# Performance work log

Measured on AMD Instinct MI355X. Metric: run time of the kernel, lower is better.

Reference implementation:

```python
import jax, jax.numpy as jnp
import numpy as np

B = 4096      # graphs per batch
V = 32        # vertices per graph
F = 16        # num_atom_types (input node features)
NB = 8        # num_bond_types (edge feature dim)
C = 128       # conv_dim
E_PER = 256   # random edges per graph
NEG_SLOPE = 0.2


def setup_inputs() -> dict:
    rng = np.random.default_rng(0)
    N = B * V
    # random intra-graph edges (duplicates are fine; softmax handles them)
    off = (np.arange(B, dtype=np.int64) * V)[:, None]
    src = (rng.integers(0, V, (B, E_PER)) + off).ravel()
    dst = (rng.integers(0, V, (B, E_PER)) + off).ravel()
    bond = rng.integers(0, NB, src.shape[0])
    eattr = np.zeros((src.shape[0], NB), dtype=np.float32)
    eattr[np.arange(src.shape[0]), bond] = 1.0
    # self loops with edge_attr = per-target-node mean (PyG fill_value='mean')
    sums = np.zeros((N, NB), dtype=np.float64)
    np.add.at(sums, dst, eattr)
    cnt = np.bincount(dst, minlength=N).astype(np.float64)
    loop_attr = (sums / np.maximum(cnt, 1.0)[:, None]).astype(np.float32)
    loops = np.arange(N, dtype=np.int64)
    edge_index = np.stack([np.concatenate([src, loops]),
                           np.concatenate([dst, loops])])  # [2, E]
    edge_attr = np.concatenate([eattr, loop_attr], axis=0)  # [E, NB]

    key = jax.random.key(0)
    ks = jax.random.split(key, 8)
    inp = {
        "x": jax.random.normal(ks[0], (N, F), jnp.float32),
        "edge_index": jnp.asarray(edge_index),
        "edge_attr": jnp.asarray(edge_attr),
        "W_lin": jax.random.normal(ks[1], (F, C), jnp.float32) / np.sqrt(F),
        "att_src": jax.random.normal(ks[2], (C,), jnp.float32) / np.sqrt(C),
        "att_dst": jax.random.normal(ks[3], (C,), jnp.float32) / np.sqrt(C),
        "att_edge": jax.random.normal(ks[4], (C,), jnp.float32) / np.sqrt(C),
        "W_edge": jax.random.normal(ks[5], (NB, C), jnp.float32) / np.sqrt(NB),
        "b_gat": jnp.zeros((C,), jnp.float32),
        "W_out": jax.random.normal(ks[6], (C, 1), jnp.float32) / np.sqrt(C),
        "b_out": jnp.zeros((1,), jnp.float32),
        "num_graphs": B,
    }
    return inp


def reference(x, edge_index, edge_attr, W_lin, att_src, att_dst, att_edge,
              W_edge, b_gat, W_out, b_out, num_graphs):
    N = x.shape[0]
    src, dst = edge_index[0], edge_index[1]
    h = x @ W_lin                           # [N, C] node transform
    a_src = h @ att_src                     # [N]
    a_dst = h @ att_dst                     # [N]
    a_edge = (edge_attr @ W_edge) @ att_edge  # [E]
    alpha = jax.nn.leaky_relu(a_src[src] + a_dst[dst] + a_edge, NEG_SLOPE)
    # segment softmax over incoming edges of each dst node
    m = jax.ops.segment_max(alpha, dst, num_segments=N)
    m = jnp.where(jnp.isfinite(m), m, 0.0)
    ex = jnp.exp(alpha - m[dst])
    denom = jax.ops.segment_sum(ex, dst, num_segments=N)
    w = ex / denom[dst]                     # [E] attention weights
    msg = h[src] * w[:, None]               # [E, C]
    out_nodes = jax.ops.segment_sum(msg, dst, num_segments=N) + b_gat  # [N, C]
    gf = out_nodes.reshape(num_graphs, -1, out_nodes.shape[-1]).mean(axis=1)  # [B, C]
    out = gf @ W_out + b_out                # [B, 1]
    return (out, gf)
```

## Files before the change

kernel.cpp:

```cpp
#include <hip/hip_runtime.h>


#define BB   4096
#define VV   32
#define FF   16
#define NBB  8
#define CC   128
#define EPER 256
constexpr int NTOT  = BB * VV;
constexpr int ERAND = BB * EPER;
constexpr int ETOT  = ERAND + NTOT;
constexpr float SLOPE = 0.2f;

__launch_bounds__(256, 4)
__global__ void gnn_all(const float* __restrict__ x,
                        const int*   __restrict__ eidx,
                        const float* __restrict__ eattr,
                        const float* __restrict__ W_lin,
                        const float* __restrict__ att_src,
                        const float* __restrict__ att_dst,
                        const float* __restrict__ att_edge,
                        const float* __restrict__ W_edge,
                        const float* __restrict__ b_gat,
                        const float* __restrict__ W_out,
                        const float* __restrict__ b_out,
                        float* __restrict__ out,
                        float* __restrict__ gf_out)
{
  const int t    = threadIdx.x;
  const int lane = t & 63;
  const int wave = __builtin_amdgcn_readfirstlane(t) >> 6;
  const int g    = blockIdx.x * 4 + wave;
  const int half = lane >> 5;
  const int v    = lane & 31;

  __shared__ float2 s_a[4][VV];
  __shared__ float  s_den[4][VV];
  __shared__ float  s_r[4][VV];
  __shared__ float2 s_uv[4][FF];
  __shared__ __align__(16) float s_we[4][NBB];
  __shared__ float  s_xt[4][FF * 33];
  __shared__ __align__(16) float s_y[4][FF];

  float4 xa, xb;
  {
    const float* xp = x + (size_t)(g * VV + v) * FF + half * 8;
    xa = ((const float4*)xp)[0]; xb = ((const float4*)xp)[1];
  }
  int es[4], ed[4];
  float4 ea0[4], ea1[4];
  #pragma unroll
  for (int k = 0; k < 4; ++k) {
    const int e = g * EPER + 64 * k + lane;
    es[k] = eidx[e] - g * VV;
    ed[k] = eidx[ETOT + e] - g * VV;
    const float4* ap = (const float4*)(eattr + (size_t)e * NBB);
    ea0[k] = ap[0]; ea1[k] = ap[1];
  }
  float4 la0 = {0,0,0,0}, la1 = {0,0,0,0};
  if (half) {
    const float4* lp = (const float4*)(eattr + (size_t)(ERAND + g * VV + v) * NBB);
    la0 = lp[0]; la1 = lp[1];
  }

  {
    const int fu = lane & 15, q = lane >> 4;
    const float4* wr = (const float4*)(W_lin + fu * CC + q * 32);
    const float4* as = (const float4*)(att_src + q * 32);
    const float4* ad = (const float4*)(att_dst + q * 32);
    float us = 0.f, ud = 0.f;
    #pragma unroll
    for (int j = 0; j < 8; ++j) {
      const float4 w = wr[j], a = as[j], d = ad[j];
      us += w.x*a.x + w.y*a.y + w.z*a.z + w.w*a.w;
      ud += w.x*d.x + w.y*d.y + w.z*d.z + w.w*d.w;
    }
    us += __shfl_xor(us, 16); us += __shfl_xor(us, 32);
    ud += __shfl_xor(ud, 16); ud += __shfl_xor(ud, 32);
    if (lane < FF) s_uv[wave][lane] = make_float2(us, ud);
  }
  if (!half) {
    const int f8 = v & 7, oct = v >> 3;
    const float4* wr = (const float4*)(W_edge + f8 * CC + oct * 32);
    const float4* ae = (const float4*)(att_edge + oct * 32);
    float pe = 0.f;
    #pragma unroll
    for (int j = 0; j < 8; ++j) {
      const float4 w = wr[j], a = ae[j];
      pe += w.x*a.x + w.y*a.y + w.z*a.z + w.w*a.w;
    }
    pe += __shfl_xor(pe, 8); pe += __shfl_xor(pe, 16);
    if (v < NBB) s_we[wave][v] = pe;
  }

  float a0 = 0.f, a1 = 0.f;
  {
    const float xr[8] = {xa.x, xa.y, xa.z, xa.w, xb.x, xb.y, xb.z, xb.w};
    #pragma unroll
    for (int j = 0; j < 8; ++j) {
      const float2 u = s_uv[wave][half * 8 + j];
      a0 += xr[j] * u.x; a1 += xr[j] * u.y;
    }
  }
  a0 += __shfl_xor(a0, 32); a1 += __shfl_xor(a1, 32);
  if (!half) {
    s_a[wave][v] = make_float2(a0, a1);
    s_den[wave][v] = 0.f; s_r[wave][v] = 0.f;
  }
  __threadfence_block();

  const float4 w03 = *(const float4*)&s_we[wave][0];
  const float4 w47 = *(const float4*)&s_we[wave][4];
  float ex[5];
  #pragma unroll
  for (int k = 0; k < 4; ++k) {
    const float2 A = s_a[wave][es[k]];
    const float2 D = s_a[wave][ed[k]];
    const float aed = ea0[k].x*w03.x + ea0[k].y*w03.y + ea0[k].z*w03.z + ea0[k].w*w03.w
                    + ea1[k].x*w47.x + ea1[k].y*w47.y + ea1[k].z*w47.z + ea1[k].w*w47.w;
    const float a  = A.x + D.y + aed;
    const float al = a > 0.f ? a : SLOPE * a;
    ex[k] = __expf(al);
    atomicAdd(&s_den[wave][ed[k]], ex[k]);
  }
  ex[4] = 0.f;
  if (half) {
    const float2 S = s_a[wave][v];
    const float aed = la0.x*w03.x + la0.y*w03.y + la0.z*w03.z + la0.w*w03.w
                    + la1.x*w47.x + la1.y*w47.y + la1.z*w47.z + la1.w*w47.w;
    const float a  = S.x + S.y + aed;
    const float al = a > 0.f ? a : SLOPE * a;
    ex[4] = __expf(al);
    atomicAdd(&s_den[wave][v], ex[4]);
  }
  __threadfence_block();

  #pragma unroll
  for (int k = 0; k < 4; ++k)
    atomicAdd(&s_r[wave][es[k]], ex[k] * __builtin_amdgcn_rcpf(s_den[wave][ed[k]]));
  if (half)
    atomicAdd(&s_r[wave][v], ex[4] * __builtin_amdgcn_rcpf(s_den[wave][v]));
  __threadfence_block();

  {
    const float rl = s_r[wave][v];
    const float xr[8] = {xa.x, xa.y, xa.z, xa.w, xb.x, xb.y, xb.z, xb.w};
    #pragma unroll
    for (int j = 0; j < 8; ++j)
      s_xt[wave][(half * 8 + j) * 33 + v] = xr[j] * rl;
  }
  __threadfence_block();
  {
    const int fy = lane & 15, part = lane >> 4;
    float yp = 0.f;
    #pragma unroll
    for (int j = 0; j < 8; ++j) yp += s_xt[wave][fy * 33 + part * 8 + j];
    yp += __shfl_xor(yp, 16); yp += __shfl_xor(yp, 32);
    if (lane < FF) s_y[wave][lane] = yp * (1.0f / VV);
  }
  __threadfence_block();

  const float4 y03 = *(const float4*)&s_y[wave][0];
  const float4 y47 = *(const float4*)&s_y[wave][4];
  const float4 y8b = *(const float4*)&s_y[wave][8];
  const float4 ycf = *(const float4*)&s_y[wave][12];
  const float yv[16] = {y03.x,y03.y,y03.z,y03.w, y47.x,y47.y,y47.z,y47.w,
                        y8b.x,y8b.y,y8b.z,y8b.w, ycf.x,ycf.y,ycf.z,ycf.w};
  const float2 bg = ((const float2*)b_gat)[lane];
  float gx = bg.x, gy = bg.y;
  const float2* W2 = (const float2*)W_lin;
  #pragma unroll
  for (int f = 0; f < FF; ++f) {
    const float2 w = W2[f * 64 + lane];
    gx += yv[f] * w.x; gy += yv[f] * w.y;
  }
  ((float2*)(gf_out + (size_t)g * CC))[lane] = make_float2(gx, gy);

  const float2 wo = ((const float2*)W_out)[lane];
  float p = gx * wo.x + gy * wo.y;
  #pragma unroll
  for (int m = 1; m <= 32; m <<= 1) p += __shfl_xor(p, m);
  if (lane == 0) out[g] = p + b_out[0];
}

extern "C" void kernel_launch(void* const* d_in, const int* in_sizes, int n_in,
                              void* d_out, int out_size, void* d_ws, size_t ws_size,
                              hipStream_t stream) {
  const float* x        = (const float*)d_in[0];
  const int*   eidx     = (const int*)  d_in[1];
  const float* eattr    = (const float*)d_in[2];
  const float* W_lin    = (const float*)d_in[3];
  const float* att_src  = (const float*)d_in[4];
  const float* att_dst  = (const float*)d_in[5];
  const float* att_edge = (const float*)d_in[6];
  const float* W_edge   = (const float*)d_in[7];
  const float* b_gat    = (const float*)d_in[8];
  const float* W_out    = (const float*)d_in[9];
  const float* b_out    = (const float*)d_in[10];

  float* out = (float*)d_out;
  float* gf  = out + BB;

  gnn_all<<<dim3(BB / 4), dim3(256), 0, stream>>>(
      x, eidx, eattr, W_lin, att_src, att_dst, att_edge, W_edge,
      b_gat, W_out, b_out, out, gf);
}
```

Measured before the change: 120.4 us.

## Process one graph per 128-thread block instead of one graph per wave

Each graph is now handled by a 128-thread block (two waves) instead of a single wave, so every thread carries half as many edges. The per-graph constant precomputation is split across the two waves. The shared-memory transpose of x times r is replaced by shuffle reductions, and the final projection gives each thread one output channel. This adds block-level __syncthreads barriers and launches four times as many blocks in exchange for more parallelism and fewer registers per thread.

```diff
diff --git a/kernel.cpp b/kernel.cpp
--- a/kernel.cpp
+++ b/kernel.cpp
@@ -12,7 +12,7 @@
 constexpr int ETOT  = ERAND + NTOT;
 constexpr float SLOPE = 0.2f;
 
-__launch_bounds__(256, 4)
+__launch_bounds__(128, 8)
 __global__ void gnn_all(const float* __restrict__ x,
                         const int*   __restrict__ eidx,
                         const float* __restrict__ eattr,
@@ -29,45 +29,43 @@
 {
   const int t    = threadIdx.x;
   const int lane = t & 63;
-  const int wave = __builtin_amdgcn_readfirstlane(t) >> 6;
-  const int g    = blockIdx.x * 4 + wave;
-  const int half = lane >> 5;
-  const int v    = lane & 31;
-
-  __shared__ float2 s_a[4][VV];
-  __shared__ float  s_den[4][VV];
-  __shared__ float  s_r[4][VV];
-  __shared__ float2 s_uv[4][FF];
-  __shared__ __align__(16) float s_we[4][NBB];
-  __shared__ float  s_xt[4][FF * 33];
-  __shared__ __align__(16) float s_y[4][FF];
-
-  float4 xa, xb;
-  {
-    const float* xp = x + (size_t)(g * VV + v) * FF + half * 8;
-    xa = ((const float4*)xp)[0]; xb = ((const float4*)xp)[1];
-  }
-  int es[4], ed[4];
-  float4 ea0[4], ea1[4];
+  const int wave = t >> 6;
+  const int g    = blockIdx.x;
+  const int r    = t >> 2;
+  const int q    = t & 3;
+
+  __shared__ float2 s_a[VV];
+  __shared__ float  s_den[VV];
+  __shared__ float  s_r[VV];
+  __shared__ float2 s_uv[FF];
+  __shared__ __align__(16) float s_we[NBB];
+  __shared__ __align__(16) float s_yp[2][FF];
+  __shared__ float  s_op[2];
+
+  const float4 xq = *(const float4*)(x + (size_t)(g * VV + r) * FF + q * 4);
+
+  int es[2], ed[2];
+  float4 ea0[2], ea1[2];
   #pragma unroll
-  for (int k = 0; k < 4; ++k) {
-    const int e = g * EPER + 64 * k + lane;
+  for (int k = 0; k < 2; ++k) {
+    const int e = g * EPER + 128 * k + t;
     es[k] = eidx[e] - g * VV;
     ed[k] = eidx[ETOT + e] - g * VV;
     const float4* ap = (const float4*)(eattr + (size_t)e * NBB);
     ea0[k] = ap[0]; ea1[k] = ap[1];
   }
+  const bool selfl = (q == 3);
   float4 la0 = {0,0,0,0}, la1 = {0,0,0,0};
-  if (half) {
-    const float4* lp = (const float4*)(eattr + (size_t)(ERAND + g * VV + v) * NBB);
+  if (selfl) {
+    const float4* lp = (const float4*)(eattr + (size_t)(ERAND + g * VV + r) * NBB);
     la0 = lp[0]; la1 = lp[1];
   }
 
-  {
-    const int fu = lane & 15, q = lane >> 4;
-    const float4* wr = (const float4*)(W_lin + fu * CC + q * 32);
-    const float4* as = (const float4*)(att_src + q * 32);
-    const float4* ad = (const float4*)(att_dst + q * 32);
+  if (wave == 0) {
+    const int fu = lane & 15, c4 = lane >> 4;
+    const float4* wr = (const float4*)(W_lin + fu * CC + c4 * 32);
+    const float4* as = (const float4*)(att_src + c4 * 32);
+    const float4* ad = (const float4*)(att_dst + c4 * 32);
     float us = 0.f, ud = 0.f;
     #pragma unroll
     for (int j = 0; j < 8; ++j) {
@@ -77,110 +75,112 @@
     }
     us += __shfl_xor(us, 16); us += __shfl_xor(us, 32);
     ud += __shfl_xor(ud, 16); ud += __shfl_xor(ud, 32);
-    if (lane < FF) s_uv[wave][lane] = make_float2(us, ud);
-  }
-  if (!half) {
-    const int f8 = v & 7, oct = v >> 3;
-    const float4* wr = (const float4*)(W_edge + f8 * CC + oct * 32);
-    const float4* ae = (const float4*)(att_edge + oct * 32);
+    if (lane < FF) s_uv[lane] = make_float2(us, ud);
+    if (lane < VV) { s_den[lane] = 0.f; s_r[lane] = 0.f; }
+  } else {
+    const int f8 = lane & 7, c16 = lane >> 3;
+    const float4* wr = (const float4*)(W_edge + f8 * CC + c16 * 16);
+    const float4* ae = (const float4*)(att_edge + c16 * 16);
     float pe = 0.f;
     #pragma unroll
-    for (int j = 0; j < 8; ++j) {
+    for (int j = 0; j < 4; ++j) {
       const float4 w = wr[j], a = ae[j];
       pe += w.x*a.x + w.y*a.y + w.z*a.z + w.w*a.w;
     }
-    pe += __shfl_xor(pe, 8); pe += __shfl_xor(pe, 16);
-    if (v < NBB) s_we[wave][v] = pe;
-  }
-
-  float a0 = 0.f, a1 = 0.f;
+    pe += __shfl_xor(pe, 8); pe += __shfl_xor(pe, 16); pe += __shfl_xor(pe, 32);
+    if (lane < NBB) s_we[lane] = pe;
+  }
+  __syncthreads();
+
+  float a0, a1;
   {
-    const float xr[8] = {xa.x, xa.y, xa.z, xa.w, xb.x, xb.y, xb.z, xb.w};
-    #pragma unroll
-    for (int j = 0; j < 8; ++j) {
-      const float2 u = s_uv[wave][half * 8 + j];
+    const float xr[4] = {xq.x, xq.y, xq.z, xq.w};
+    a0 = 0.f; a1 = 0.f;
+    #pragma unroll
+    for (int j = 0; j < 4; ++j) {
+      const float2 u = s_uv[q * 4 + j];
       a0 += xr[j] * u.x; a1 += xr[j] * u.y;
     }
   }
-  a0 += __shfl_xor(a0, 32); a1 += __shfl_xor(a1, 32);
-  if (!half) {
-    s_a[wave][v] = make_float2(a0, a1);
-    s_den[wave][v] = 0.f; s_r[wave][v] = 0.f;
-  }
-  __threadfence_block();
-
-  const float4 w03 = *(const float4*)&s_we[wave][0];
-  const float4 w47 = *(const float4*)&s_we[wave][4];
-  float ex[5];
+  a0 += __shfl_xor(a0, 1); a0 += __shfl_xor(a0, 2);
+  a1 += __shfl_xor(a1, 1); a1 += __shfl_xor(a1, 2);
+  if (q == 0) s_a[r] = make_float2(a0, a1);
+  __syncthreads();
+
+  const float4 w03 = *(const float4*)&s_we[0];
+  const float4 w47 = *(const float4*)&s_we[4];
+  float ex[2], exl = 0.f;
   #pragma unroll
-  for (int k = 0; k < 4; ++k) {
-    const float2 A = s_a[wave][es[k]];
-    const float2 D = s_a[wave][ed[k]];
+  for (int k = 0; k < 2; ++k) {
+    const float2 A = s_a[es[k]];
+    const float2 D = s_a[ed[k]];
     const float aed = ea0[k].x*w03.x + ea0[k].y*w03.y + ea0[k].z*w03.z + ea0[k].w*w03.w
                     + ea1[k].x*w47.x + ea1[k].y*w47.y + ea1[k].z*w47.z + ea1[k].w*w47.w;
     const float a  = A.x + D.y + aed;
     const float al = a > 0.f ? a : SLOPE * a;
     ex[k] = __expf(al);
-    atomicAdd(&s_den[wave][ed[k]], ex[k]);
-  }
-  ex[4] = 0.f;
-  if (half) {
-    const float2 S = s_a[wave][v];
+    atomicAdd(&s_den[ed[k]], ex[k]);
+  }
+  if (selfl) {
+    const float2 S = s_a[r];
     const float aed = la0.x*w03.x + la0.y*w03.y + la0.z*w03.z + la0.w*w03.w
                     + la1.x*w47.x + la1.y*w47.y + la1.z*w47.z + la1.w*w47.w;
     const float a  = S.x + S.y + aed;
     const float al = a > 0.f ? a : SLOPE * a;
-    ex[4] = __expf(al);
-    atomicAdd(&s_den[wave][v], ex[4]);
-  }
-  __threadfence_block();
+    exl = __expf(al);
+    atomicAdd(&s_den[r], exl);
+  }
+  __syncthreads();
 
   #pragma unroll
-  for (int k = 0; k < 4; ++k)
-    atomicAdd(&s_r[wave][es[k]], ex[k] * __builtin_amdgcn_rcpf(s_den[wave][ed[k]]));
-  if (half)
-    atomicAdd(&s_r[wave][v], ex[4] * __builtin_amdgcn_rcpf(s_den[wave][v]));
-  __threadfence_block();
+  for (int k = 0; k < 2; ++k)
+    atomicAdd(&s_r[es[k]], ex[k] * __builtin_amdgcn_rcpf(s_den[ed[k]]));
+  if (selfl)
+    atomicAdd(&s_r[r], exl * __builtin_amdgcn_rcpf(s_den[r]));
+  __syncthreads();
 
   {
-    const float rl = s_r[wave][v];
-    const float xr[8] = {xa.x, xa.y, xa.z, xa.w, xb.x, xb.y, xb.z, xb.w};
-    #pragma unroll
-    for (int j = 0; j < 8; ++j)
-      s_xt[wave][(half * 8 + j) * 33 + v] = xr[j] * rl;
-  }
-  __threadfence_block();
+    const float rl = s_r[r];
+    float v0 = xq.x * rl, v1 = xq.y * rl, v2 = xq.z * rl, v3 = xq.w * rl;
+    #pragma unroll
+    for (int m = 4; m <= 32; m <<= 1) {
+      v0 += __shfl_xor(v0, m); v1 += __shfl_xor(v1, m);
+      v2 += __shfl_xor(v2, m); v3 += __shfl_xor(v3, m);
+    }
+    if (lane < 4)
+      *(float4*)&s_yp[wave][lane * 4] = make_float4(v0, v1, v2, v3);
+  }
+  __syncthreads();
+
   {
-    const int fy = lane & 15, part = lane >> 4;
-    float yp = 0.f;
-    #pragma unroll
-    for (int j = 0; j < 8; ++j) yp += s_xt[wave][fy * 33 + part * 8 + j];
-    yp += __shfl_xor(yp, 16); yp += __shfl_xor(yp, 32);
-    if (lane < FF) s_y[wave][lane] = yp * (1.0f / VV);
-  }
-  __threadfence_block();
-
-  const float4 y03 = *(const float4*)&s_y[wave][0];
-  const float4 y47 = *(const float4*)&s_y[wave][4];
-  const float4 y8b = *(const float4*)&s_y[wave][8];
-  const float4 ycf = *(const float4*)&s_y[wave][12];
-  const float yv[16] = {y03.x,y03.y,y03.z,y03.w, y47.x,y47.y,y47.z,y47.w,
-                        y8b.x,y8b.y,y8b.z,y8b.w, ycf.x,ycf.y,ycf.z,ycf.w};
-  const float2 bg = ((const float2*)b_gat)[lane];
-  float gx = bg.x, gy = bg.y;
-  const float2* W2 = (const float2*)W_lin;
-  #pragma unroll
-  for (int f = 0; f < FF; ++f) {
-    const float2 w = W2[f * 64 + lane];
-    gx += yv[f] * w.x; gy += yv[f] * w.y;
-  }
-  ((float2*)(gf_out + (size_t)g * CC))[lane] = make_float2(gx, gy);
-
-  const float2 wo = ((const float2*)W_out)[lane];
-  float p = gx * wo.x + gy * wo.y;
-  #pragma unroll
-  for (int m = 1; m <= 32; m <<= 1) p += __shfl_xor(p, m);
-  if (lane == 0) out[g] = p + b_out[0];
+    const int c = t;
+    const float4 p0 = ((const float4*)&s_yp[0][0])[0];
+    const float4 p1 = ((const float4*)&s_yp[0][0])[1];
+    const float4 p2 = ((const float4*)&s_yp[0][0])[2];
+    const float4 p3 = ((const float4*)&s_yp[0][0])[3];
+    const float4 r0 = ((const float4*)&s_yp[1][0])[0];
+    const float4 r1 = ((const float4*)&s_yp[1][0])[1];
+    const float4 r2 = ((const float4*)&s_yp[1][0])[2];
+    const float4 r3 = ((const float4*)&s_yp[1][0])[3];
+    const float yv[16] = {
+      p0.x+r0.x, p0.y+r0.y, p0.z+r0.z, p0.w+r0.w,
+      p1.x+r1.x, p1.y+r1.y, p1.z+r1.z, p1.w+r1.w,
+      p2.x+r2.x, p2.y+r2.y, p2.z+r2.z, p2.w+r2.w,
+      p3.x+r3.x, p3.y+r3.y, p3.z+r3.z, p3.w+r3.w };
+    float gacc = 0.f;
+    #pragma unroll
+    for (int f = 0; f < FF; ++f)
+      gacc += yv[f] * W_lin[f * CC + c];
+    const float gf = b_gat[c] + gacc * (1.0f / VV);
+    gf_out[(size_t)g * CC + c] = gf;
+
+    float p = gf * W_out[c];
+    #pragma unroll
+    for (int m = 1; m <= 32; m <<= 1) p += __shfl_xor(p, m);
+    if (lane == 0) s_op[wave] = p;
+  }
+  __syncthreads();
+  if (t == 0) out[g] = s_op[0] + s_op[1] + b_out[0];
 }
 
 extern "C" void kernel_launch(void* const* d_in, const int* in_sizes, int n_in,
@@ -201,7 +201,7 @@
   float* out = (float*)d_out;
   float* gf  = out + BB;
 
-  gnn_all<<<dim3(BB / 4), dim3(256), 0, stream>>>(
+  gnn_all<<<dim3(BB), dim3(128), 0, stream>>>(
       x, eidx, eattr, W_lin, att_src, att_dst, att_edge, W_edge,
       b_gat, W_out, b_out, out, gf);
 }
```

New measurement: 135.3 us. 1.12x slower.
